# Kernel tuning notes

Measured on AMD Instinct MI355X. Metric: run time of the kernel, lower is better.

The kernel has to match this reference:

```python
import jax, jax.numpy as jnp
import numpy as np

MARGIN = 0.1

def setup_inputs() -> dict:
    key = jax.random.key(0)
    k1, k2 = jax.random.split(key)
    embeddings = jax.random.normal(k1, (8192, 128), dtype=jnp.float32)
    labels = jax.random.randint(k2, (8192,), 0, 64, dtype=jnp.int64)
    return {"embeddings": embeddings, "labels": labels}

def reference(embeddings, labels):
    # sim[i,j] = <e_i, e_j>
    sim = embeddings @ embeddings.T  # [n, n]
    eq = labels[:, None] == labels[None, :]  # pos mask (includes diagonal)
    # per entry: exp(margin - sim) for positives, exp(sim - margin) for negatives
    terms = jnp.where(eq, jnp.exp(MARGIN - sim), jnp.exp(sim - MARGIN))
    # loss_i = log(sum_j terms[i,j]); loss = mean_i loss_i
    return jnp.mean(jnp.log(jnp.sum(terms, axis=1)))
```

## Files before the change

### kernel.cpp

```cpp
#include <hip/hip_runtime.h>
#include <hip/hip_bf16.h>

#define N 8192
#define D 128
#define LOG2E  1.44269504088896f
#define LN2    0.69314718055995f

typedef __attribute__((ext_vector_type(8))) short bf16x8;
typedef __attribute__((ext_vector_type(4))) float f32x4;

#if __has_builtin(__builtin_amdgcn_exp2f)
#define EXP2(x) __builtin_amdgcn_exp2f(x)
#else
#define EXP2(x) exp2f(x)
#endif
#if __has_builtin(__builtin_amdgcn_logf)
#define LOG2(x) __builtin_amdgcn_logf(x)
#else
#define LOG2(x) log2f(x)
#endif

static __device__ __forceinline__ unsigned short f2bf(float f) {
    union { float f; unsigned int u; } x;
    x.f = f;
    unsigned int r = ((x.u >> 16) & 1u) + 0x7FFFu;
    return (unsigned short)((x.u + r) >> 16);
}

__global__ void prep_kernel(const float* __restrict__ E,
                            uint4* __restrict__ Eb2,
                            unsigned int* __restrict__ counter) {
    const int j = blockIdx.x * 256 + threadIdx.x;
    const int l  = j & 15;
    const int q  = (j >> 4) & 3;
    const int kk = (j >> 6) & 3;
    const int S  = j >> 8;
    const float4* src = (const float4*)(E + (size_t)(S * 16 + l) * D + kk * 32 + q * 8);
    float4 f0 = src[0], f1 = src[1];
    uint4 o;
    o.x = f2bf(f0.x) | ((unsigned)f2bf(f0.y) << 16);
    o.y = f2bf(f0.z) | ((unsigned)f2bf(f0.w) << 16);
    o.z = f2bf(f1.x) | ((unsigned)f2bf(f1.y) << 16);
    o.w = f2bf(f1.z) | ((unsigned)f2bf(f1.w) << 16);
    Eb2[j] = o;
    if (j == 0) *counter = 0u;
}

__global__ __launch_bounds__(256) void fused_kernel(
        const unsigned short* __restrict__ Eb2,
        const int* __restrict__ labels,
        float* __restrict__ part) {
    __shared__ int   labC[128];
    __shared__ int   labR[128];
    __shared__ float colacc[128];

    const int tid  = threadIdx.x;
    const int wid  = tid >> 6;
    const int lane = tid & 63;
    const int q = lane >> 4;
    const int l = lane & 15;

    const int b = blockIdx.x;
    int r = (int)(64.5f - sqrtf(64.5f * 64.5f - 2.0f * (float)b));
    while ((r + 1) * 64 - ((r + 1) * r) / 2 <= b) ++r;
    while (r * 64 - (r * (r - 1)) / 2 > b) --r;
    const int c = r + (b - (r * 64 - (r * (r - 1)) / 2));
    const bool diag = (r == c);
    const int tile_m0 = r * 128;
    const int n_begin = c * 128;
    const int mrow0 = wid * 32;

    const char* base = (const char*)Eb2;

    bf16x8 a[2][4];
#pragma unroll
    for (int g = 0; g < 2; ++g) {
        const char* pa = base + (size_t)(r * 8 + wid * 2 + g) * 4096 + lane * 16;
#pragma unroll
        for (int kk = 0; kk < 4; ++kk)
            a[g][kk] = *(const bf16x8*)(pa + kk * 1024);
    }

    if (tid < 128) { labC[tid] = labels[n_begin + tid]; colacc[tid] = 0.0f; }
    else           { labR[tid - 128] = labels[tile_m0 + (tid - 128)]; }
    __syncthreads();

    int lrow[8];
#pragma unroll
    for (int g = 0; g < 2; ++g)
#pragma unroll
        for (int rr = 0; rr < 4; ++rr)
            lrow[g * 4 + rr] = labR[mrow0 + g * 16 + q * 4 + rr];

    float sum[8];
#pragma unroll
    for (int i = 0; i < 8; ++i) sum[i] = 0.0f;

#pragma clang loop unroll(disable)
    for (int s = 0; s < 8; ++s) {
        const char* pb = base + (size_t)(c * 8 + s) * 4096 + lane * 16;
        bf16x8 b0 = *(const bf16x8*)(pb);
        bf16x8 b1 = *(const bf16x8*)(pb + 1024);
        bf16x8 b2 = *(const bf16x8*)(pb + 2048);
        bf16x8 b3 = *(const bf16x8*)(pb + 3072);
        const int lc = labC[s * 16 + l];

        f32x4 acc0 = (f32x4){0.f, 0.f, 0.f, 0.f};
        f32x4 acc1 = (f32x4){0.f, 0.f, 0.f, 0.f};
        acc0 = __builtin_amdgcn_mfma_f32_16x16x32_bf16(a[0][0], b0, acc0, 0, 0, 0);
        acc0 = __builtin_amdgcn_mfma_f32_16x16x32_bf16(a[0][1], b1, acc0, 0, 0, 0);
        acc0 = __builtin_amdgcn_mfma_f32_16x16x32_bf16(a[0][2], b2, acc0, 0, 0, 0);
        acc0 = __builtin_amdgcn_mfma_f32_16x16x32_bf16(a[0][3], b3, acc0, 0, 0, 0);
        acc1 = __builtin_amdgcn_mfma_f32_16x16x32_bf16(a[1][0], b0, acc1, 0, 0, 0);
        acc1 = __builtin_amdgcn_mfma_f32_16x16x32_bf16(a[1][1], b1, acc1, 0, 0, 0);
        acc1 = __builtin_amdgcn_mfma_f32_16x16x32_bf16(a[1][2], b2, acc1, 0, 0, 0);
        acc1 = __builtin_amdgcn_mfma_f32_16x16x32_bf16(a[1][3], b3, acc1, 0, 0, 0);

        float cp = 0.0f;
#pragma unroll
        for (int g = 0; g < 2; ++g) {
#pragma unroll
            for (int rr = 0; rr < 4; ++rr) {
                float sv = (g == 0) ? acc0[rr] : acc1[rr];
                bool eq = (lrow[g * 4 + rr] == lc);
                float cc = eq ? -LOG2E : LOG2E;
                float term = EXP2(cc * (sv - 0.1f));
                sum[g * 4 + rr] += term;
                cp += term;
            }
        }
        if (!diag) {
            cp += __shfl_xor(cp, 16);
            cp += __shfl_xor(cp, 32);
            if (q == 0) atomicAdd(&colacc[s * 16 + l], cp);
        }
    }

#pragma unroll
    for (int i = 0; i < 8; ++i) {
        float v = sum[i];
        v += __shfl_xor(v, 1);
        v += __shfl_xor(v, 2);
        v += __shfl_xor(v, 4);
        v += __shfl_xor(v, 8);
        sum[i] = v;
    }
    if (l == 0) {
#pragma unroll
        for (int g = 0; g < 2; ++g)
#pragma unroll
            for (int rr = 0; rr < 4; ++rr)
                part[(size_t)c * N + tile_m0 + mrow0 + g * 16 + q * 4 + rr] = sum[g * 4 + rr];
    }

    __syncthreads();
    if (!diag && tid < 128)
        part[(size_t)r * N + n_begin + tid] = colacc[tid];
}

__global__ void finalize_kernel(const float* __restrict__ part,
                                float* __restrict__ bpart,
                                unsigned int* __restrict__ counter,
                                float* __restrict__ out) {
    __shared__ float red[4];
    __shared__ unsigned int tk;
    const int tid = threadIdx.x;
    const int i = blockIdx.x * 256 + tid;

    float s = 0.0f;
#pragma unroll 8
    for (int x = 0; x < 64; ++x) s += part[(size_t)x * N + i];
    float v = LOG2(s) * LN2;
#pragma unroll
    for (int off = 1; off <= 32; off <<= 1) v += __shfl_xor(v, off);
    if ((tid & 63) == 0) red[tid >> 6] = v;
    __syncthreads();
    if (tid == 0) {
        bpart[blockIdx.x] = red[0] + red[1] + red[2] + red[3];
        __threadfence();
        tk = atomicAdd(counter, 1u);
    }
    __syncthreads();
    if (tk == 31u) {
        __threadfence();
        if (tid < 64) {
            float t = (tid < 32)
                ? __hip_atomic_load(&bpart[tid], __ATOMIC_RELAXED,
                                    __HIP_MEMORY_SCOPE_AGENT)
                : 0.0f;
#pragma unroll
            for (int off = 1; off <= 32; off <<= 1) t += __shfl_xor(t, off);
            if (tid == 0) out[0] = t * (1.0f / (float)N);
        }
    }
}

extern "C" void kernel_launch(void* const* d_in, const int* in_sizes, int n_in,
                              void* d_out, int out_size, void* d_ws, size_t ws_size,
                              hipStream_t stream) {
    const float* E = (const float*)d_in[0];
    const int* labels = (const int*)d_in[1];
    float* out = (float*)d_out;

    unsigned short* Eb2 = (unsigned short*)d_ws;
    float* part = (float*)((char*)d_ws + (size_t)N * D * 2);
    float* bpart = part + (size_t)64 * N;
    unsigned int* counter = (unsigned int*)(bpart + 32);

    prep_kernel<<<512, 256, 0, stream>>>(E, (uint4*)Eb2, counter);
    fused_kernel<<<2080, 256, 0, stream>>>(Eb2, labels, part);
    finalize_kernel<<<32, 256, 0, stream>>>(part, bpart, counter, out);
}
```

Before: 85.07 us.

## Stage B tile in LDS via direct loads and accumulate row sums atomically

```diff
diff --git a/kernel.cpp b/kernel.cpp
--- a/kernel.cpp
+++ b/kernel.cpp
@@ -20,6 +20,9 @@
 #define LOG2(x) log2f(x)
 #endif
 
+typedef const __attribute__((address_space(1))) unsigned int as1_u32c;
+typedef __attribute__((address_space(3))) unsigned int as3_u32;
+
 static __device__ __forceinline__ unsigned short f2bf(float f) {
     union { float f; unsigned int u; } x;
     x.f = f;
@@ -29,7 +32,7 @@
 
 __global__ void prep_kernel(const float* __restrict__ E,
                             uint4* __restrict__ Eb2,
-                            unsigned int* __restrict__ counter) {
+                            float* __restrict__ rowsum) {
     const int j = blockIdx.x * 256 + threadIdx.x;
     const int l  = j & 15;
     const int q  = (j >> 4) & 3;
@@ -43,13 +46,14 @@
     o.z = f2bf(f1.x) | ((unsigned)f2bf(f1.y) << 16);
     o.w = f2bf(f1.z) | ((unsigned)f2bf(f1.w) << 16);
     Eb2[j] = o;
-    if (j == 0) *counter = 0u;
+    if (j < N) rowsum[j] = 0.0f;
 }
 
 __global__ __launch_bounds__(256) void fused_kernel(
         const unsigned short* __restrict__ Eb2,
         const int* __restrict__ labels,
-        float* __restrict__ part) {
+        float* __restrict__ rowsum) {
+    __shared__ uint4 btile4[2048];
     __shared__ int   labC[128];
     __shared__ int   labR[128];
     __shared__ float colacc[128];
@@ -71,6 +75,7 @@
     const int mrow0 = wid * 32;
 
     const char* base = (const char*)Eb2;
+    char* bt = (char*)btile4;
 
     bf16x8 a[2][4];
 #pragma unroll
@@ -81,8 +86,21 @@
             a[g][kk] = *(const bf16x8*)(pa + kk * 1024);
     }
 
+    {
+        const char* gB = base + (size_t)(c * 8) * 4096;
+#pragma unroll
+        for (int u = 0; u < 8; ++u) {
+            const int m = wid * 8 + u;
+            __builtin_amdgcn_global_load_lds(
+                (as1_u32c*)(gB + m * 1024 + lane * 16),
+                (as3_u32*)(bt + m * 1024),
+                16, 0, 0);
+        }
+    }
+
     if (tid < 128) { labC[tid] = labels[n_begin + tid]; colacc[tid] = 0.0f; }
     else           { labR[tid - 128] = labels[tile_m0 + (tid - 128)]; }
+    asm volatile("s_waitcnt vmcnt(0)" ::: "memory");
     __syncthreads();
 
     int lrow[8];
@@ -98,7 +116,7 @@
 
 #pragma clang loop unroll(disable)
     for (int s = 0; s < 8; ++s) {
-        const char* pb = base + (size_t)(c * 8 + s) * 4096 + lane * 16;
+        const char* pb = bt + s * 4096 + lane * 16;
         bf16x8 b0 = *(const bf16x8*)(pb);
         bf16x8 b1 = *(const bf16x8*)(pb + 1024);
         bf16x8 b2 = *(const bf16x8*)(pb + 2048);
@@ -150,49 +168,29 @@
         for (int g = 0; g < 2; ++g)
 #pragma unroll
             for (int rr = 0; rr < 4; ++rr)
-                part[(size_t)c * N + tile_m0 + mrow0 + g * 16 + q * 4 + rr] = sum[g * 4 + rr];
+                atomicAdd(&rowsum[tile_m0 + mrow0 + g * 16 + q * 4 + rr],
+                          sum[g * 4 + rr]);
     }
 
     __syncthreads();
     if (!diag && tid < 128)
-        part[(size_t)r * N + n_begin + tid] = colacc[tid];
-}
-
-__global__ void finalize_kernel(const float* __restrict__ part,
-                                float* __restrict__ bpart,
-                                unsigned int* __restrict__ counter,
+        atomicAdd(&rowsum[n_begin + tid], colacc[tid]);
+}
+
+__global__ void finalize_kernel(const float* __restrict__ rowsum,
                                 float* __restrict__ out) {
     __shared__ float red[4];
-    __shared__ unsigned int tk;
     const int tid = threadIdx.x;
-    const int i = blockIdx.x * 256 + tid;
-
-    float s = 0.0f;
+    float v = 0.0f;
 #pragma unroll 8
-    for (int x = 0; x < 64; ++x) s += part[(size_t)x * N + i];
-    float v = LOG2(s) * LN2;
+    for (int k = 0; k < 32; ++k) v += LOG2(rowsum[tid + 256 * k]);
+    v *= LN2;
 #pragma unroll
     for (int off = 1; off <= 32; off <<= 1) v += __shfl_xor(v, off);
     if ((tid & 63) == 0) red[tid >> 6] = v;
     __syncthreads();
-    if (tid == 0) {
-        bpart[blockIdx.x] = red[0] + red[1] + red[2] + red[3];
-        __threadfence();
-        tk = atomicAdd(counter, 1u);
-    }
-    __syncthreads();
-    if (tk == 31u) {
-        __threadfence();
-        if (tid < 64) {
-            float t = (tid < 32)
-                ? __hip_atomic_load(&bpart[tid], __ATOMIC_RELAXED,
-                                    __HIP_MEMORY_SCOPE_AGENT)
-                : 0.0f;
-#pragma unroll
-            for (int off = 1; off <= 32; off <<= 1) t += __shfl_xor(t, off);
-            if (tid == 0) out[0] = t * (1.0f / (float)N);
-        }
-    }
+    if (tid == 0)
+        out[0] = (red[0] + red[1] + red[2] + red[3]) * (1.0f / (float)N);
 }
 
 extern "C" void kernel_launch(void* const* d_in, const int* in_sizes, int n_in,
@@ -203,11 +201,9 @@
     float* out = (float*)d_out;
 
     unsigned short* Eb2 = (unsigned short*)d_ws;
-    float* part = (float*)((char*)d_ws + (size_t)N * D * 2);
-    float* bpart = part + (size_t)64 * N;
-    unsigned int* counter = (unsigned int*)(bpart + 32);
-
-    prep_kernel<<<512, 256, 0, stream>>>(E, (uint4*)Eb2, counter);
-    fused_kernel<<<2080, 256, 0, stream>>>(Eb2, labels, part);
-    finalize_kernel<<<32, 256, 0, stream>>>(part, bpart, counter, out);
-}
+    float* rowsum = (float*)((char*)d_ws + (size_t)N * D * 2);
+
+    prep_kernel<<<512, 256, 0, stream>>>(E, (uint4*)Eb2, rowsum);
+    fused_kernel<<<2080, 256, 0, stream>>>(Eb2, labels, rowsum);
+    finalize_kernel<<<1, 256, 0, stream>>>(rowsum, out);
+}
```

New measurement: 86.72 us. No clear change (+1.9%).
